# Kernel tuning notes

Hardware: AMD Instinct MI355X
Metric: run time of the kernel (lower is better)

## Reference

```python
import jax, jax.numpy as jnp
import numpy as np

D_MODEL, D_K, D_V, H, D_FF = 512, 64, 64, 8, 2048
B, N = 8, 1024
LN_EPS = 1e-5


def _layer_norm(x, g, b):
    mu = jnp.mean(x, axis=-1, keepdims=True)
    var = jnp.mean((x - mu) ** 2, axis=-1, keepdims=True)
    return (x - mu) * jax.lax.rsqrt(var + LN_EPS) * g + b


def setup_inputs() -> dict:
    key = jax.random.key(0)
    ks = jax.random.split(key, 16)
    s = 0.02
    return {
        "queries": jax.random.normal(ks[0], (B, N, D_MODEL), jnp.float32),
        "keys": jax.random.normal(ks[1], (B, N, D_MODEL), jnp.float32),
        "values": jax.random.normal(ks[2], (B, N, D_MODEL), jnp.float32),
        "relative_geometry_weights": jax.random.uniform(ks[3], (B, H, N, N), jnp.float32),
        "pos": jax.random.normal(ks[4], (B, N, D_MODEL), jnp.float32),
        "Wq": jax.random.normal(ks[5], (D_MODEL, H * D_K), jnp.float32) * s,
        "bq": jnp.zeros((H * D_K,), jnp.float32),
        "Wk": jax.random.normal(ks[6], (D_MODEL, H * D_K), jnp.float32) * s,
        "bk": jnp.zeros((H * D_K,), jnp.float32),
        "Wv": jax.random.normal(ks[7], (D_MODEL, H * D_V), jnp.float32) * s,
        "bv": jnp.zeros((H * D_V,), jnp.float32),
        "Wo": jax.random.normal(ks[8], (H * D_V, D_MODEL), jnp.float32) * s,
        "bo": jnp.zeros((D_MODEL,), jnp.float32),
        "ln1_g": jnp.ones((D_MODEL,), jnp.float32),
        "ln1_b": jnp.zeros((D_MODEL,), jnp.float32),
        "W1": jax.random.normal(ks[9], (D_MODEL, D_FF), jnp.float32) * s,
        "b1": jnp.zeros((D_FF,), jnp.float32),
        "W2": jax.random.normal(ks[10], (D_FF, D_MODEL), jnp.float32) * s,
        "b2": jnp.zeros((D_MODEL,), jnp.float32),
        "ln2_g": jnp.ones((D_MODEL,), jnp.float32),
        "ln2_b": jnp.zeros((D_MODEL,), jnp.float32),
    }


def reference(queries, keys, values, relative_geometry_weights, pos,
              Wq, bq, Wk, bk, Wv, bv, Wo, bo, ln1_g, ln1_b,
              W1, b1, W2, b2, ln2_g, ln2_b):
    b, n, _ = queries.shape
    # positional injection on q/k only
    q_in = queries + pos
    k_in = keys + pos
    # projections -> [b, h, n, d]
    q = (q_in @ Wq + bq).reshape(b, n, H, D_K).transpose(0, 2, 1, 3)
    k = (k_in @ Wk + bk).reshape(b, n, H, D_K).transpose(0, 2, 1, 3)
    v = (values @ Wv + bv).reshape(b, n, H, D_V).transpose(0, 2, 1, 3)
    # scaled dot-product scores with geometry bias: log(clamp(w_g)) + scores
    att = jnp.einsum('bhqd,bhkd->bhqk', q, k) / jnp.sqrt(jnp.float32(D_K))
    w_mn = jnp.log(jnp.clip(relative_geometry_weights, 1e-6, None)) + att
    w_mn = jax.nn.softmax(w_mn, axis=-1)
    out = jnp.einsum('bhqk,bhkd->bhqd', w_mn, v)  # [b,h,n,d_v]
    out = out.transpose(0, 2, 1, 3).reshape(b, n, H * D_V) @ Wo + bo
    # residual + layernorm (dropout is identity in eval)
    att_out = _layer_norm(queries + out, ln1_g, ln1_b)
    # position-wise FFN with residual + layernorm
    ff = jax.nn.relu(att_out @ W1 + b1) @ W2 + b2
    return _layer_norm(att_out + ff, ln2_g, ln2_b)
```

## Files before the change

### kernel.cpp

```cpp
#include <hip/hip_runtime.h>
#include <hip/hip_bf16.h>
#include <stdint.h>

#define B_   8
#define N_   1024
#define DM   512
#define H_   8
#define DFF  2048
#define ROWS (B_ * N_)
#define QKV_LD (3 * DM)
#define LOG2E 1.4426950408889634f
#define SCL  (0.125f * LOG2E)

typedef __bf16 bf16x8 __attribute__((ext_vector_type(8)));
typedef float  f32x4  __attribute__((ext_vector_type(4)));

__device__ __forceinline__ void gld_lds16(const void* g, void* l) {
  __builtin_amdgcn_global_load_lds((__attribute__((address_space(1))) void*)g,
                                   (__attribute__((address_space(3))) void*)l, 16, 0, 0);
}

__device__ __forceinline__ unsigned short bfb(float x) {
  __bf16 h = (__bf16)x;
  unsigned short u;
  __builtin_memcpy(&u, &h, 2);
  return u;
}

__global__ __launch_bounds__(256) void prep_and_wt(
    const float* __restrict__ q, const float* __restrict__ k,
    const float* __restrict__ v, const float* __restrict__ pos,
    __bf16* __restrict__ xq, __bf16* __restrict__ xk, __bf16* __restrict__ xv,
    const float* __restrict__ Wq, const float* __restrict__ Wk,
    const float* __restrict__ Wv, const float* __restrict__ Wo,
    const float* __restrict__ W1, const float* __restrict__ W2,
    __bf16* __restrict__ WqkvT, __bf16* __restrict__ WoT,
    __bf16* __restrict__ W1T, __bf16* __restrict__ W2T) {
  __shared__ float tl[32][33];
  if (blockIdx.x < 4096) {
    int i = blockIdx.x * 256 + threadIdx.x;
    float4 pv = ((const float4*)pos)[i];
    float4 qv = ((const float4*)q)[i];
    float4 kv = ((const float4*)k)[i];
    float4 vv = ((const float4*)v)[i];
    ushort4 o;
    o.x = bfb(qv.x + pv.x); o.y = bfb(qv.y + pv.y); o.z = bfb(qv.z + pv.z); o.w = bfb(qv.w + pv.w);
    ((ushort4*)xq)[i] = o;
    o.x = bfb(kv.x + pv.x); o.y = bfb(kv.y + pv.y); o.z = bfb(kv.z + pv.z); o.w = bfb(kv.w + pv.w);
    ((ushort4*)xk)[i] = o;
    o.x = bfb(vv.x); o.y = bfb(vv.y); o.z = bfb(vv.z); o.w = bfb(vv.w);
    ((ushort4*)xv)[i] = o;
    return;
  }
  int idx = blockIdx.x - 4096;
  const float* src; __bf16* dst; int K, N, t;
  if (idx < 768) {
    src = idx < 256 ? Wq : (idx < 512 ? Wk : Wv);
    dst = WqkvT + (size_t)(idx >> 8) * 512 * 512;
    K = 512; N = 512; t = idx & 255;
  } else if (idx < 1024) { src = Wo; dst = WoT;  K = 512;  N = 512;  t = idx - 768; }
  else if (idx < 2048)   { src = W1; dst = W1T;  K = 512;  N = 2048; t = idx - 1024; }
  else                   { src = W2; dst = W2T;  K = 2048; N = 512;  t = idx - 2048; }
  int tiles_n = N >> 5;
  int tn = t & (tiles_n - 1), tk = t / tiles_n;
  int n0 = tn * 32, k0 = tk * 32;
  int x = threadIdx.x & 31, y4 = threadIdx.x >> 5;
  #pragma unroll
  for (int j = y4; j < 32; j += 8) tl[j][x] = src[(size_t)(k0 + j) * N + n0 + x];
  __syncthreads();
  #pragma unroll
  for (int j = y4; j < 32; j += 8)
    dst[(size_t)(n0 + j) * K + k0 + x] = (__bf16)tl[x][j];
}

template <int EPI, int BN>
__global__ __launch_bounds__(256, 2) void gemm_bt(
    const __bf16* __restrict__ A0, const __bf16* __restrict__ A1, const __bf16* __restrict__ A2,
    const __bf16* __restrict__ BT,
    const float* __restrict__ bias0, const float* __restrict__ bias1, const float* __restrict__ bias2,
    void* __restrict__ Cp, __bf16* __restrict__ Vtp, int M, int N, int K, int nsplit) {
  constexpr int NFR = BN / 32;
  constexpr int WCW = BN / 2;
  constexpr int BI  = BN / 32;
  __shared__ __align__(16) __bf16 As[128 * 64];
  __shared__ __align__(16) __bf16 Bs[BN * 64];
  int tid = threadIdx.x, lane = tid & 63;
  int wave = tid >> 6;
  int wr = (wave >> 1) * 64, wc = (wave & 1) * WCW;

  int gx = N / BN;
  int nwg = gridDim.x;
  int cpx = nwg >> 3;
  int swz = (blockIdx.x & 7) * cpx + (blockIdx.x >> 3);
  int bx = swz % gx, by = swz / gx;
  int row0 = by << 7, col0 = bx * BN;

  int asel = col0 / nsplit;
  const __bf16* A = asel == 0 ? A0 : (asel == 1 ? A1 : A2);
  const float* bias = asel == 0 ? bias0 : (asel == 1 ? bias1 : bias2);

  f32x4 acc[4][NFR] = {};

  for (int kt = 0; kt < K; kt += 64) {
    #pragma unroll
    for (int i = 0; i < 4; ++i) {
      int t = i * 256 + tid;
      int r = t >> 3, cL = t & 7;
      int cS = cL ^ (r & 7);
      gld_lds16(A + (size_t)(row0 + r) * K + kt + cS * 8, As + t * 8);
    }
    #pragma unroll
    for (int i = 0; i < BI; ++i) {
      int t = i * 256 + tid;
      int r = t >> 3, cL = t & 7;
      int cS = cL ^ (r & 7);
      gld_lds16(BT + (size_t)(col0 + r) * K + kt + cS * 8, Bs + t * 8);
    }
    __syncthreads();
    #pragma unroll
    for (int ks = 0; ks < 2; ++ks) {
      bf16x8 af[4], bfr[NFR];
      #pragma unroll
      for (int m = 0; m < 4; ++m) {
        int r = wr + m * 16 + (lane & 15);
        int c = (ks * 4 + (lane >> 4)) ^ (r & 7);
        af[m] = *(const bf16x8*)(As + r * 64 + c * 8);
      }
      #pragma unroll
      for (int n = 0; n < NFR; ++n) {
        int r = wc + n * 16 + (lane & 15);
        int c = (ks * 4 + (lane >> 4)) ^ (r & 7);
        bfr[n] = *(const bf16x8*)(Bs + r * 64 + c * 8);
      }
      #pragma unroll
      for (int m = 0; m < 4; ++m)
        #pragma unroll
        for (int n = 0; n < NFR; ++n)
          acc[m][n] = __builtin_amdgcn_mfma_f32_16x16x32_bf16(af[m], bfr[n], acc[m][n], 0, 0, 0);
    }
    __syncthreads();
  }

  int rb = row0 + wr + ((lane >> 4) << 2);
  int cb = col0 + wc + (lane & 15);
  if (EPI == 3 && asel == 2) {
    int bb = row0 >> 10;
    #pragma unroll
    for (int n = 0; n < NFR; ++n) {
      int c = cb + n * 16;
      int d = c & 63, hh = (c >> 6) & 7;
      float bv = bias[c % nsplit];
      size_t vbase = ((size_t)((bb * 8 + hh) * 64 + d)) << 10;
      #pragma unroll
      for (int m = 0; m < 4; ++m) {
        int r0 = (rb + m * 16) & 1023;
        ushort4 pk;
        pk.x = bfb(acc[m][n][0] + bv);
        pk.y = bfb(acc[m][n][1] + bv);
        pk.z = bfb(acc[m][n][2] + bv);
        pk.w = bfb(acc[m][n][3] + bv);
        *(ushort4*)((__bf16*)Vtp + vbase + r0) = pk;
      }
    }
    return;
  }
  #pragma unroll
  for (int n = 0; n < NFR; ++n) {
    int c = cb + n * 16;
    float bv = bias[c % nsplit];
    #pragma unroll
    for (int m = 0; m < 4; ++m) {
      #pragma unroll
      for (int j = 0; j < 4; ++j) {
        int r = rb + m * 16 + j;
        float v = acc[m][n][j] + bv;
        if (EPI == 1) v = fmaxf(v, 0.f);
        if (EPI == 2) ((float*)Cp)[(size_t)r * N + c] = v;
        else          ((__bf16*)Cp)[(size_t)r * N + c] = (__bf16)v;
      }
    }
  }
}

__global__ __launch_bounds__(256, 3) void attn_kernel(
    const __bf16* __restrict__ QKV, const __bf16* __restrict__ Vt,
    const float* __restrict__ rgw, __bf16* __restrict__ O) {
  __shared__ __align__(16) __bf16 Qs[64 * 64];
  __shared__ __align__(16) __bf16 Ks[2][64 * 64];
  __shared__ __align__(16) __bf16 Vs[2][64 * 64];
  __shared__ __align__(16) __bf16 Ps[4][16 * 64];

  int tid = threadIdx.x, lane = tid & 63, wave = tid >> 6;
  int flat = (blockIdx.x & 7) * 128 + (blockIdx.x >> 3);
  int qt = flat & 15, h = (flat >> 4) & 7, b = flat >> 7;
  int q0 = qt * 64;
  const int g = lane >> 4, u = lane & 15;

  const float* rgw_p = rgw +
      ((size_t)(b * H_ + h) * N_ + (size_t)(q0 + wave * 16 + u)) * N_ + g * 4;

#define STAGE_KV(BUF, KT)                                                      \
  {                                                                            \
    _Pragma("unroll")                                                          \
    for (int i = 0; i < 2; ++i) {                                              \
      int t = i * 256 + tid;                                                   \
      int r = t >> 3, cL = t & 7, cS = cL ^ (r & 7);                           \
      gld_lds16(QKV + (size_t)(b * N_ + (KT) + r) * QKV_LD + DM + h * 64 + cS * 8, Ks[BUF] + t * 8); \
      gld_lds16(Vt + (size_t)((b * H_ + h) * 64 + r) * N_ + (KT) + cS * 8, Vs[BUF] + t * 8);         \
    }                                                                          \
  }
#define RPF(W, T)                                                              \
  {                                                                            \
    _Pragma("unroll")                                                          \
    for (int n = 0; n < 4; ++n)                                                \
      W[n] = __builtin_nontemporal_load((const f32x4*)(rgw_p + (size_t)(T) * 64 + n * 16)); \
  }

  #pragma unroll
  for (int i = 0; i < 2; ++i) {
    int t = i * 256 + tid;
    int r = t >> 3, cL = t & 7, cS = cL ^ (r & 7);
    gld_lds16(QKV + (size_t)(b * N_ + q0 + r) * QKV_LD + h * 64 + cS * 8, Qs + t * 8);
  }
  STAGE_KV(0, 0)
  __builtin_amdgcn_sched_barrier(0);
  f32x4 wA[4], wB[4], wC[4], wD[4];
  RPF(wA, 0) RPF(wB, 1) RPF(wC, 2)
  __builtin_amdgcn_sched_barrier(0);

  float l = 0.f;
  f32x4 oacc[4] = {};
  bf16x8 qf[2];
  __bf16* pw = &Ps[wave][0];

  union Pk { __bf16 h4[4]; unsigned long long q; };

#define PHASE(T16, WAITSTR, DOSTAGE, DORPF, WCON, WPF)                         \
  {                                                                            \
    asm volatile(WAITSTR ::: "memory");                                        \
    __builtin_amdgcn_s_barrier();                                              \
    if (DOSTAGE) { STAGE_KV(((T16) + 1) & 1, ((T16) + 1) * 64) }               \
    __builtin_amdgcn_sched_barrier(0);                                         \
    if (DORPF) { RPF(WPF, (T16) + 3) }                                         \
    __builtin_amdgcn_sched_barrier(0);                                         \
    if ((T16) == 0) {                                                          \
      int r = wave * 16 + u;                                                   \
      _Pragma("unroll")                                                        \
      for (int ks = 0; ks < 2; ++ks) {                                         \
        int c = (ks * 4 + g) ^ (r & 7);                                        \
        qf[ks] = *(const bf16x8*)(Qs + r * 64 + c * 8);                        \
      }                                                                        \
    }                                                                          \
    f32x4 s[4] = {};                                                           \
    __builtin_amdgcn_s_setprio(1);                                             \
    _Pragma("unroll")                                                          \
    for (int ks = 0; ks < 2; ++ks) {                                           \
      _Pragma("unroll")                                                        \
      for (int n = 0; n < 4; ++n) {                                            \
        int r = n * 16 + u;                                                    \
        int c = (ks * 4 + g) ^ (r & 7);                                        \
        bf16x8 kf = *(const bf16x8*)(Ks[(T16) & 1] + r * 64 + c * 8);          \
        s[n] = __builtin_amdgcn_mfma_f32_16x16x32_bf16(kf, qf[ks], s[n], 0, 0, 0); \
      }                                                                        \
    }                                                                          \
    __builtin_amdgcn_s_setprio(0);                                             \
    _Pragma("unroll")                                                          \
    for (int n = 0; n < 4; ++n) {                                              \
      Pk pk;                                                                   \
      _Pragma("unroll")                                                        \
      for (int j = 0; j < 4; ++j) {                                            \
        float pv = fmaxf(WCON[n][j], 1e-6f) * exp2f(s[n][j] * SCL);            \
        l += pv;                                                               \
        pk.h4[j] = (__bf16)pv;                                                 \
      }                                                                        \
      int bcol = 2 * n + (g >> 1);                                             \
      *(unsigned long long*)(pw + u * 64 + ((bcol ^ (u & 7)) << 3) + ((g & 1) << 2)) = pk.q; \
    }                                                                          \
    __builtin_amdgcn_s_setprio(1);                                             \
    _Pragma("unroll")                                                          \
    for (int ks = 0; ks < 2; ++ks) {                                           \
      int cp = (ks * 4 + g) ^ (u & 7);                                         \
      bf16x8 pa = *(const bf16x8*)(pw + u * 64 + cp * 8);                      \
      _Pragma("unroll")                                                        \
      for (int n = 0; n < 4; ++n) {                                            \
        int r = n * 16 + u;                                                    \
        int c = (ks * 4 + g) ^ (r & 7);                                        \
        bf16x8 vb = *(const bf16x8*)(Vs[(T16) & 1] + r * 64 + c * 8);          \
        oacc[n] = __builtin_amdgcn_mfma_f32_16x16x32_bf16(pa, vb, oacc[n], 0, 0, 0); \
      }                                                                        \
    }                                                                          \
    __builtin_amdgcn_s_setprio(0);                                             \
  }

  PHASE(0,  "s_waitcnt vmcnt(12)", 1, 1, wA, wD)
  PHASE(1,  "s_waitcnt vmcnt(4)",  1, 1, wB, wA)
  PHASE(2,  "s_waitcnt vmcnt(4)",  1, 1, wC, wB)
  PHASE(3,  "s_waitcnt vmcnt(4)",  1, 1, wD, wC)
  PHASE(4,  "s_waitcnt vmcnt(4)",  1, 1, wA, wD)
  PHASE(5,  "s_waitcnt vmcnt(4)",  1, 1, wB, wA)
  PHASE(6,  "s_waitcnt vmcnt(4)",  1, 1, wC, wB)
  PHASE(7,  "s_waitcnt vmcnt(4)",  1, 1, wD, wC)
  PHASE(8,  "s_waitcnt vmcnt(4)",  1, 1, wA, wD)
  PHASE(9,  "s_waitcnt vmcnt(4)",  1, 1, wB, wA)
  PHASE(10, "s_waitcnt vmcnt(4)",  1, 1, wC, wB)
  PHASE(11, "s_waitcnt vmcnt(4)",  1, 1, wD, wC)
  PHASE(12, "s_waitcnt vmcnt(4)",  1, 1, wA, wD)
  PHASE(13, "s_waitcnt vmcnt(4)",  1, 0, wB, wA)
  PHASE(14, "s_waitcnt vmcnt(0)",  1, 0, wC, wB)
  PHASE(15, "s_waitcnt vmcnt(0)",  0, 0, wD, wC)
#undef PHASE
#undef STAGE_KV
#undef RPF

  l += __shfl_xor(l, 16);
  l += __shfl_xor(l, 32);
  float linv[4];
  #pragma unroll
  for (int j = 0; j < 4; ++j)
    linv[j] = 1.f / __shfl(l, (lane & 48) | (g * 4 + j));

  int orow = b * N_ + q0 + wave * 16 + g * 4;
  int ocol = h * 64 + u;
  #pragma unroll
  for (int j = 0; j < 4; ++j)
    #pragma unroll
    for (int n = 0; n < 4; ++n)
      O[(size_t)(orow + j) * DM + ocol + n * 16] = (__bf16)(oacc[n][j] * linv[j]);
}

template <int WRITE_BF>
__global__ __launch_bounds__(256) void ln_kernel(
    const float* __restrict__ x1, const float* __restrict__ x2,
    const float* __restrict__ gw, const float* __restrict__ bw,
    float* __restrict__ outf, __bf16* __restrict__ outb) {
  __shared__ float red[8];
  int row = blockIdx.x, t = threadIdx.x;
  size_t base = (size_t)row * DM;
  float v0 = x1[base + t] + x2[base + t];
  float v1 = x1[base + t + 256] + x2[base + t + 256];
  float s = v0 + v1, s2 = v0 * v0 + v1 * v1;
  #pragma unroll
  for (int o = 32; o; o >>= 1) { s += __shfl_xor(s, o); s2 += __shfl_xor(s2, o); }
  int wave = t >> 6;
  if ((t & 63) == 0) { red[wave] = s; red[4 + wave] = s2; }
  __syncthreads();
  s = red[0] + red[1] + red[2] + red[3];
  s2 = red[4] + red[5] + red[6] + red[7];
  float mu = s * (1.f / DM);
  float var = s2 * (1.f / DM) - mu * mu;
  float rstd = rsqrtf(var + 1e-5f);
  float y0 = (v0 - mu) * rstd * gw[t] + bw[t];
  float y1 = (v1 - mu) * rstd * gw[t + 256] + bw[t + 256];
  outf[base + t] = y0;
  outf[base + t + 256] = y1;
  if (WRITE_BF) {
    outb[base + t] = (__bf16)y0;
    outb[base + t + 256] = (__bf16)y1;
  }
}

extern "C" void kernel_launch(void* const* d_in, const int* in_sizes, int n_in,
                              void* d_out, int out_size, void* d_ws, size_t ws_size,
                              hipStream_t stream) {
  const float* queries = (const float*)d_in[0];
  const float* keys    = (const float*)d_in[1];
  const float* values  = (const float*)d_in[2];
  const float* rgw     = (const float*)d_in[3];
  const float* pos     = (const float*)d_in[4];
  const float* Wq = (const float*)d_in[5];
  const float* bq = (const float*)d_in[6];
  const float* Wk = (const float*)d_in[7];
  const float* bk = (const float*)d_in[8];
  const float* Wv = (const float*)d_in[9];
  const float* bv = (const float*)d_in[10];
  const float* Wo = (const float*)d_in[11];
  const float* bo = (const float*)d_in[12];
  const float* ln1g = (const float*)d_in[13];
  const float* ln1b = (const float*)d_in[14];
  const float* W1 = (const float*)d_in[15];
  const float* b1 = (const float*)d_in[16];
  const float* W2 = (const float*)d_in[17];
  const float* b2 = (const float*)d_in[18];
  const float* ln2g = (const float*)d_in[19];
  const float* ln2b = (const float*)d_in[20];
  float* out = (float*)d_out;

  char* ws = (char*)d_ws;
  const size_t SZX = (size_t)ROWS * DM * 2;
  __bf16* Xq    = (__bf16*)(ws);
  __bf16* Xk    = (__bf16*)(ws + SZX);
  __bf16* Xv    = (__bf16*)(ws + 2 * SZX);
  __bf16* WqkvT = (__bf16*)(ws + 3 * SZX);
  __bf16* WoT   = (__bf16*)(ws + 3 * SZX + 1572864);
  __bf16* W1T   = (__bf16*)(ws + 3 * SZX + 2097152);
  __bf16* W2T   = (__bf16*)(ws + 3 * SZX + 4194304);
  __bf16* QKV   = (__bf16*)(ws + 3 * SZX + 6291456);
  __bf16* Vt    = (__bf16*)(ws + 3 * SZX + 6291456 + 3 * SZX);
  __bf16* Oat   = (__bf16*)(ws + 3 * SZX + 6291456 + 4 * SZX);
  float*  attproj = (float*)Xq;
  __bf16* attoutb = Xv;
  float*  attoutf = (float*)QKV;
  float*  ff2     = (float*)Vt;
  __bf16* ff1     = (__bf16*)(ws + 3 * SZX + 6291456 + 5 * SZX);

  prep_and_wt<<<4096 + 3072, 256, 0, stream>>>(
      queries, keys, values, pos, Xq, Xk, Xv,
      Wq, Wk, Wv, Wo, W1, W2, WqkvT, WoT, W1T, W2T);

  gemm_bt<3, 128><<<(ROWS / 128) * (QKV_LD / 128), 256, 0, stream>>>(
      Xq, Xk, Xv, WqkvT, bq, bk, bv, QKV, Vt, ROWS, QKV_LD, DM, DM);

  attn_kernel<<<B_ * H_ * (N_ / 64), 256, 0, stream>>>(QKV, Vt, rgw, Oat);

  gemm_bt<2, 64><<<(ROWS / 128) * (DM / 64), 256, 0, stream>>>(
      Oat, Oat, Oat, WoT, bo, bo, bo, attproj, nullptr, ROWS, DM, DM, DM);

  ln_kernel<1><<<ROWS, 256, 0, stream>>>(queries, attproj, ln1g, ln1b, attoutf, attoutb);

  gemm_bt<1, 128><<<(ROWS / 128) * (DFF / 128), 256, 0, stream>>>(
      attoutb, attoutb, attoutb, W1T, b1, b1, b1, ff1, nullptr, ROWS, DFF, DM, DFF);

  gemm_bt<2, 64><<<(ROWS / 128) * (DM / 64), 256, 0, stream>>>(
      ff1, ff1, ff1, W2T, b2, b2, b2, ff2, nullptr, ROWS, DM, DFF, DM);

  ln_kernel<0><<<ROWS, 256, 0, stream>>>(attoutf, ff2, ln2g, ln2b, out, nullptr);
}
```

Measured before the change: 223.6 us.

## Load K/V fragments directly into registers, dropping LDS staging and barriers

```diff
diff --git a/kernel.cpp b/kernel.cpp
--- a/kernel.cpp
+++ b/kernel.cpp
@@ -182,12 +182,10 @@
   }
 }
 
-__global__ __launch_bounds__(256, 3) void attn_kernel(
+__global__ __launch_bounds__(256, 2) void attn_kernel(
     const __bf16* __restrict__ QKV, const __bf16* __restrict__ Vt,
     const float* __restrict__ rgw, __bf16* __restrict__ O) {
   __shared__ __align__(16) __bf16 Qs[64 * 64];
-  __shared__ __align__(16) __bf16 Ks[2][64 * 64];
-  __shared__ __align__(16) __bf16 Vs[2][64 * 64];
   __shared__ __align__(16) __bf16 Ps[4][16 * 64];
 
   int tid = threadIdx.x, lane = tid & 63, wave = tid >> 6;
@@ -196,25 +194,27 @@
   int q0 = qt * 64;
   const int g = lane >> 4, u = lane & 15;
 
-  const float* rgw_p = rgw +
+  const __bf16* kbase = QKV + (size_t)(b * N_ + u) * QKV_LD + DM + h * 64 + g * 8;
+  const __bf16* vbase = Vt + (size_t)((b * H_ + h) * 64 + u) * N_ + g * 8;
+  const float*  rgw_p = rgw +
       ((size_t)(b * H_ + h) * N_ + (size_t)(q0 + wave * 16 + u)) * N_ + g * 4;
 
-#define STAGE_KV(BUF, KT)                                                      \
-  {                                                                            \
-    _Pragma("unroll")                                                          \
-    for (int i = 0; i < 2; ++i) {                                              \
-      int t = i * 256 + tid;                                                   \
-      int r = t >> 3, cL = t & 7, cS = cL ^ (r & 7);                           \
-      gld_lds16(QKV + (size_t)(b * N_ + (KT) + r) * QKV_LD + DM + h * 64 + cS * 8, Ks[BUF] + t * 8); \
-      gld_lds16(Vt + (size_t)((b * H_ + h) * 64 + r) * N_ + (KT) + cS * 8, Vs[BUF] + t * 8);         \
-    }                                                                          \
-  }
-#define RPF(W, T)                                                              \
-  {                                                                            \
-    _Pragma("unroll")                                                          \
+#define LOADK(KF, T)                                                           \
+  { _Pragma("unroll")                                                          \
+    for (int ks = 0; ks < 2; ++ks)                                             \
+      _Pragma("unroll")                                                        \
+      for (int n = 0; n < 4; ++n)                                              \
+        KF[ks][n] = *(const bf16x8*)(kbase + (size_t)((T) * 64 + n * 16) * QKV_LD + ks * 32); }
+#define LOADV(VF, T)                                                           \
+  { _Pragma("unroll")                                                          \
+    for (int ks = 0; ks < 2; ++ks)                                             \
+      _Pragma("unroll")                                                        \
+      for (int n = 0; n < 4; ++n)                                              \
+        VF[ks][n] = *(const bf16x8*)(vbase + (size_t)(n * 16) * N_ + (T) * 64 + ks * 32); }
+#define LOADW(W, T)                                                            \
+  { _Pragma("unroll")                                                          \
     for (int n = 0; n < 4; ++n)                                                \
-      W[n] = __builtin_nontemporal_load((const f32x4*)(rgw_p + (size_t)(T) * 64 + n * 16)); \
-  }
+      W[n] = __builtin_nontemporal_load((const f32x4*)(rgw_p + (size_t)(T) * 64 + n * 16)); }
 
   #pragma unroll
   for (int i = 0; i < 2; ++i) {
@@ -222,48 +222,41 @@
     int r = t >> 3, cL = t & 7, cS = cL ^ (r & 7);
     gld_lds16(QKV + (size_t)(b * N_ + q0 + r) * QKV_LD + h * 64 + cS * 8, Qs + t * 8);
   }
-  STAGE_KV(0, 0)
-  __builtin_amdgcn_sched_barrier(0);
-  f32x4 wA[4], wB[4], wC[4], wD[4];
-  RPF(wA, 0) RPF(wB, 1) RPF(wC, 2)
-  __builtin_amdgcn_sched_barrier(0);
+  bf16x8 kfA[2][4], kfB[2][4], vfA[2][4], vfB[2][4];
+  f32x4 wA[4], wB[4], wC[4];
+  LOADK(kfA, 0) LOADV(vfA, 0)
+  LOADW(wA, 0) LOADW(wB, 1) LOADW(wC, 2)
+  __syncthreads();
+  bf16x8 qf[2];
+  {
+    int r = wave * 16 + u;
+    #pragma unroll
+    for (int ks = 0; ks < 2; ++ks) {
+      int c = (ks * 4 + g) ^ (r & 7);
+      qf[ks] = *(const bf16x8*)(Qs + r * 64 + c * 8);
+    }
+  }
 
   float l = 0.f;
   f32x4 oacc[4] = {};
-  bf16x8 qf[2];
   __bf16* pw = &Ps[wave][0];
-
   union Pk { __bf16 h4[4]; unsigned long long q; };
 
-#define PHASE(T16, WAITSTR, DOSTAGE, DORPF, WCON, WPF)                         \
+#define PHASE(T, KC, KN, VC, VN, WCON, DOK, DOV, DOW)                          \
   {                                                                            \
-    asm volatile(WAITSTR ::: "memory");                                        \
-    __builtin_amdgcn_s_barrier();                                              \
-    if (DOSTAGE) { STAGE_KV(((T16) + 1) & 1, ((T16) + 1) * 64) }               \
-    __builtin_amdgcn_sched_barrier(0);                                         \
-    if (DORPF) { RPF(WPF, (T16) + 3) }                                         \
-    __builtin_amdgcn_sched_barrier(0);                                         \
-    if ((T16) == 0) {                                                          \
-      int r = wave * 16 + u;                                                   \
-      _Pragma("unroll")                                                        \
-      for (int ks = 0; ks < 2; ++ks) {                                         \
-        int c = (ks * 4 + g) ^ (r & 7);                                        \
-        qf[ks] = *(const bf16x8*)(Qs + r * 64 + c * 8);                        \
-      }                                                                        \
-    }                                                                          \
+                         \
     f32x4 s[4] = {};                                                           \
     __builtin_amdgcn_s_setprio(1);                                             \
     _Pragma("unroll")                                                          \
-    for (int ks = 0; ks < 2; ++ks) {                                           \
+    for (int ks = 0; ks < 2; ++ks)                                             \
       _Pragma("unroll")                                                        \
-      for (int n = 0; n < 4; ++n) {                                            \
-        int r = n * 16 + u;                                                    \
-        int c = (ks * 4 + g) ^ (r & 7);                                        \
-        bf16x8 kf = *(const bf16x8*)(Ks[(T16) & 1] + r * 64 + c * 8);          \
-        s[n] = __builtin_amdgcn_mfma_f32_16x16x32_bf16(kf, qf[ks], s[n], 0, 0, 0); \
-      }                                                                        \
-    }                                                                          \
+      for (int n = 0; n < 4; ++n)                                              \
+        s[n] = __builtin_amdgcn_mfma_f32_16x16x32_bf16(KC[ks][n], qf[ks], s[n], 0, 0, 0); \
     __builtin_amdgcn_s_setprio(0);                                             \
+    __builtin_amdgcn_sched_barrier(0);                                         \
+    if (DOK) { LOADK(KN, (T) + 1) }                                            \
+    __builtin_amdgcn_sched_barrier(0);                                         \
+                           \
     _Pragma("unroll")                                                          \
     for (int n = 0; n < 4; ++n) {                                              \
       Pk pk;                                                                   \
@@ -276,41 +269,45 @@
       int bcol = 2 * n + (g >> 1);                                             \
       *(unsigned long long*)(pw + u * 64 + ((bcol ^ (u & 7)) << 3) + ((g & 1) << 2)) = pk.q; \
     }                                                                          \
+    __builtin_amdgcn_sched_barrier(0);                                         \
+    if (DOW) { LOADW(WCON, (T) + 3) }                                          \
+    __builtin_amdgcn_sched_barrier(0);                                         \
+                                                               \
     __builtin_amdgcn_s_setprio(1);                                             \
     _Pragma("unroll")                                                          \
     for (int ks = 0; ks < 2; ++ks) {                                           \
       int cp = (ks * 4 + g) ^ (u & 7);                                         \
       bf16x8 pa = *(const bf16x8*)(pw + u * 64 + cp * 8);                      \
       _Pragma("unroll")                                                        \
-      for (int n = 0; n < 4; ++n) {                                            \
-        int r = n * 16 + u;                                                    \
-        int c = (ks * 4 + g) ^ (r & 7);                                        \
-        bf16x8 vb = *(const bf16x8*)(Vs[(T16) & 1] + r * 64 + c * 8);          \
-        oacc[n] = __builtin_amdgcn_mfma_f32_16x16x32_bf16(pa, vb, oacc[n], 0, 0, 0); \
-      }                                                                        \
+      for (int n = 0; n < 4; ++n)                                              \
+        oacc[n] = __builtin_amdgcn_mfma_f32_16x16x32_bf16(pa, VC[ks][n], oacc[n], 0, 0, 0); \
     }                                                                          \
     __builtin_amdgcn_s_setprio(0);                                             \
-  }
-
-  PHASE(0,  "s_waitcnt vmcnt(12)", 1, 1, wA, wD)
-  PHASE(1,  "s_waitcnt vmcnt(4)",  1, 1, wB, wA)
-  PHASE(2,  "s_waitcnt vmcnt(4)",  1, 1, wC, wB)
-  PHASE(3,  "s_waitcnt vmcnt(4)",  1, 1, wD, wC)
-  PHASE(4,  "s_waitcnt vmcnt(4)",  1, 1, wA, wD)
-  PHASE(5,  "s_waitcnt vmcnt(4)",  1, 1, wB, wA)
-  PHASE(6,  "s_waitcnt vmcnt(4)",  1, 1, wC, wB)
-  PHASE(7,  "s_waitcnt vmcnt(4)",  1, 1, wD, wC)
-  PHASE(8,  "s_waitcnt vmcnt(4)",  1, 1, wA, wD)
-  PHASE(9,  "s_waitcnt vmcnt(4)",  1, 1, wB, wA)
-  PHASE(10, "s_waitcnt vmcnt(4)",  1, 1, wC, wB)
-  PHASE(11, "s_waitcnt vmcnt(4)",  1, 1, wD, wC)
-  PHASE(12, "s_waitcnt vmcnt(4)",  1, 1, wA, wD)
-  PHASE(13, "s_waitcnt vmcnt(4)",  1, 0, wB, wA)
-  PHASE(14, "s_waitcnt vmcnt(0)",  1, 0, wC, wB)
-  PHASE(15, "s_waitcnt vmcnt(0)",  0, 0, wD, wC)
+    __builtin_amdgcn_sched_barrier(0);                                         \
+    if (DOV) { LOADV(VN, (T) + 1) }                                            \
+    __builtin_amdgcn_sched_barrier(0);                                         \
+  }
+
+  PHASE(0,  kfA, kfB, vfA, vfB, wA, 1, 1, 1)
+  PHASE(1,  kfB, kfA, vfB, vfA, wB, 1, 1, 1)
+  PHASE(2,  kfA, kfB, vfA, vfB, wC, 1, 1, 1)
+  PHASE(3,  kfB, kfA, vfB, vfA, wA, 1, 1, 1)
+  PHASE(4,  kfA, kfB, vfA, vfB, wB, 1, 1, 1)
+  PHASE(5,  kfB, kfA, vfB, vfA, wC, 1, 1, 1)
+  PHASE(6,  kfA, kfB, vfA, vfB, wA, 1, 1, 1)
+  PHASE(7,  kfB, kfA, vfB, vfA, wB, 1, 1, 1)
+  PHASE(8,  kfA, kfB, vfA, vfB, wC, 1, 1, 1)
+  PHASE(9,  kfB, kfA, vfB, vfA, wA, 1, 1, 1)
+  PHASE(10, kfA, kfB, vfA, vfB, wB, 1, 1, 1)
+  PHASE(11, kfB, kfA, vfB, vfA, wC, 1, 1, 1)
+  PHASE(12, kfA, kfB, vfA, vfB, wA, 1, 1, 1)
+  PHASE(13, kfB, kfA, vfB, vfA, wB, 1, 1, 0)
+  PHASE(14, kfA, kfB, vfA, vfB, wC, 1, 1, 0)
+  PHASE(15, kfB, kfA, vfB, vfA, wA, 0, 0, 0)
 #undef PHASE
-#undef STAGE_KV
-#undef RPF
+#undef LOADK
+#undef LOADV
+#undef LOADW
 
   l += __shfl_xor(l, 16);
   l += __shfl_xor(l, 32);
```

After: 285.1 us. +27.5%, slower.

## Double-buffer GEMM LDS tiles to overlap global loads with MFMA compute

Applied to the files above, without the earlier changes.

```diff
diff --git a/kernel.cpp b/kernel.cpp
--- a/kernel.cpp
+++ b/kernel.cpp
@@ -82,8 +82,8 @@
   constexpr int NFR = BN / 32;
   constexpr int WCW = BN / 2;
   constexpr int BI  = BN / 32;
-  __shared__ __align__(16) __bf16 As[128 * 64];
-  __shared__ __align__(16) __bf16 Bs[BN * 64];
+  __shared__ __align__(16) __bf16 As[2][128 * 64];
+  __shared__ __align__(16) __bf16 Bs[2][BN * 64];
   int tid = threadIdx.x, lane = tid & 63;
   int wave = tid >> 6;
   int wr = (wave >> 1) * 64, wc = (wave & 1) * WCW;
@@ -101,45 +101,63 @@
 
   f32x4 acc[4][NFR] = {};
 
-  for (int kt = 0; kt < K; kt += 64) {
-    #pragma unroll
-    for (int i = 0; i < 4; ++i) {
-      int t = i * 256 + tid;
-      int r = t >> 3, cL = t & 7;
-      int cS = cL ^ (r & 7);
-      gld_lds16(A + (size_t)(row0 + r) * K + kt + cS * 8, As + t * 8);
-    }
-    #pragma unroll
-    for (int i = 0; i < BI; ++i) {
-      int t = i * 256 + tid;
-      int r = t >> 3, cL = t & 7;
-      int cS = cL ^ (r & 7);
-      gld_lds16(BT + (size_t)(col0 + r) * K + kt + cS * 8, Bs + t * 8);
-    }
-    __syncthreads();
-    #pragma unroll
-    for (int ks = 0; ks < 2; ++ks) {
-      bf16x8 af[4], bfr[NFR];
-      #pragma unroll
-      for (int m = 0; m < 4; ++m) {
-        int r = wr + m * 16 + (lane & 15);
-        int c = (ks * 4 + (lane >> 4)) ^ (r & 7);
-        af[m] = *(const bf16x8*)(As + r * 64 + c * 8);
-      }
-      #pragma unroll
-      for (int n = 0; n < NFR; ++n) {
-        int r = wc + n * 16 + (lane & 15);
-        int c = (ks * 4 + (lane >> 4)) ^ (r & 7);
-        bfr[n] = *(const bf16x8*)(Bs + r * 64 + c * 8);
-      }
-      #pragma unroll
-      for (int m = 0; m < 4; ++m)
-        #pragma unroll
-        for (int n = 0; n < NFR; ++n)
-          acc[m][n] = __builtin_amdgcn_mfma_f32_16x16x32_bf16(af[m], bfr[n], acc[m][n], 0, 0, 0);
-    }
-    __syncthreads();
-  }
+#define GSTAGE(BUF, KT)                                                        \
+  { _Pragma("unroll")                                                          \
+    for (int i = 0; i < 4; ++i) {                                              \
+      int t = i * 256 + tid;                                                   \
+      int r = t >> 3, cS = (t & 7) ^ (r & 7);                                  \
+      gld_lds16(A + (size_t)(row0 + r) * K + (KT) + cS * 8, As[BUF] + t * 8);  \
+    }                                                                          \
+    _Pragma("unroll")                                                          \
+    for (int i = 0; i < BI; ++i) {                                             \
+      int t = i * 256 + tid;                                                   \
+      int r = t >> 3, cS = (t & 7) ^ (r & 7);                                  \
+      gld_lds16(BT + (size_t)(col0 + r) * K + (KT) + cS * 8, Bs[BUF] + t * 8); \
+    } }
+
+#define GCOMP(BUF)                                                             \
+  { const __bf16* Asc = As[BUF];                                               \
+    const __bf16* Bsc = Bs[BUF];                                               \
+    _Pragma("unroll")                                                          \
+    for (int ks = 0; ks < 2; ++ks) {                                           \
+      bf16x8 af[4], bfr[NFR];                                                  \
+      _Pragma("unroll")                                                        \
+      for (int m = 0; m < 4; ++m) {                                            \
+        int r = wr + m * 16 + (lane & 15);                                     \
+        int c = (ks * 4 + (lane >> 4)) ^ (r & 7);                              \
+        af[m] = *(const bf16x8*)(Asc + r * 64 + c * 8);                        \
+      }                                                                        \
+      _Pragma("unroll")                                                        \
+      for (int n = 0; n < NFR; ++n) {                                          \
+        int r = wc + n * 16 + (lane & 15);                                     \
+        int c = (ks * 4 + (lane >> 4)) ^ (r & 7);                              \
+        bfr[n] = *(const bf16x8*)(Bsc + r * 64 + c * 8);                       \
+      }                                                                        \
+      _Pragma("unroll")                                                        \
+      for (int m = 0; m < 4; ++m)                                              \
+        _Pragma("unroll")                                                      \
+        for (int n = 0; n < NFR; ++n)                                          \
+          acc[m][n] = __builtin_amdgcn_mfma_f32_16x16x32_bf16(af[m], bfr[n], acc[m][n], 0, 0, 0); \
+    } }
+
+  GSTAGE(0, 0)
+  int cur = 0;
+  for (int kt = 64; kt < K; kt += 64) {
+    GSTAGE(cur ^ 1, kt)
+    if constexpr (BN == 128) asm volatile("s_waitcnt vmcnt(8)" ::: "memory");
+    else                     asm volatile("s_waitcnt vmcnt(6)" ::: "memory");
+    __builtin_amdgcn_s_barrier();
+    __builtin_amdgcn_sched_barrier(0);
+    GCOMP(cur)
+    __builtin_amdgcn_s_barrier();
+    cur ^= 1;
+  }
+  asm volatile("s_waitcnt vmcnt(0)" ::: "memory");
+  __builtin_amdgcn_s_barrier();
+  __builtin_amdgcn_sched_barrier(0);
+  GCOMP(cur)
+#undef GSTAGE
+#undef GCOMP
 
   int rb = row0 + wr + ((lane >> 4) << 2);
   int cb = col0 + wc + (lane & 15);
```

After: 223.9 us. Within noise of the previous version (+0.1%).
